# Kernel tuning notes

Hardware: AMD Instinct MI355X
Metric: run time of the kernel (lower is better)

## Reference

```python
import jax, jax.numpy as jnp
import numpy as np

NUM_HEADS = 6
WIN = 16
NW = 16   # number of windows sharing one mask (b_ % NW == 0)


def setup_inputs() -> dict:
    key = jax.random.key(0)
    ks = jax.random.split(key, 6)
    b_, n, dim = 256, WIN * WIN, 192
    qkv = jax.random.normal(ks[0], (b_, n, 3 * dim), dtype=jnp.float32)
    rpi = jax.random.randint(ks[1], (n, n), 0, (2 * WIN - 1) * (2 * WIN - 1))
    # additive attention mask per window-group (Swin uses 0 / -100; randn is fine for math)
    mask = jax.random.normal(ks[2], (NW, n, n), dtype=jnp.float32)
    rpb_table = 0.02 * jax.random.normal(ks[3], ((2 * WIN - 1) * (2 * WIN - 1), NUM_HEADS), dtype=jnp.float32)
    proj_w = jax.random.normal(ks[4], (dim, dim), dtype=jnp.float32) * (1.0 / np.sqrt(dim))
    proj_b = jax.random.normal(ks[5], (dim,), dtype=jnp.float32) * 0.01
    return {"qkv": qkv, "rpi": rpi, "mask": mask, "rpb_table": rpb_table,
            "proj_w": proj_w, "proj_b": proj_b}


def reference(qkv, rpi, mask, rpb_table, proj_w, proj_b):
    b_, n, c3 = qkv.shape
    c = c3 // 3
    h = NUM_HEADS
    hd = c // h
    scale = float(hd) ** -0.5
    # (b_, n, 3, h, hd) -> (3, b_, h, n, hd)
    qkv = qkv.reshape(b_, n, 3, h, hd).transpose(2, 0, 3, 1, 4)
    q, k, v = qkv[0] * scale, qkv[1], qkv[2]
    attn = jnp.einsum('bhqd,bhkd->bhqk', q, k)  # [b_, h, n, n]
    # gathered relative position bias: [n, n, h] -> [h, n, n]
    bias = rpb_table[rpi].transpose(2, 0, 1)
    attn = attn + bias[None]
    # add per-window-group mask: [b_//nw, nw, h, n, n]
    nw = mask.shape[0]
    attn = attn.reshape(b_ // nw, nw, h, n, n) + mask[None, :, None]
    attn = attn.reshape(b_, h, n, n)
    attn = jax.nn.softmax(attn, axis=-1)
    x = jnp.einsum('bhqk,bhkd->bhqd', attn, v)  # [b_, h, n, hd]
    x = x.transpose(0, 2, 1, 3).reshape(b_, n, c)
    # nn.Linear: x @ W^T + b
    return x @ proj_w.T + proj_b
```

## Files before the change

### kernel.cpp

```cpp
#include <hip/hip_runtime.h>
#include <hip/hip_bf16.h>

typedef _Float16 f16;
typedef _Float16 f16x2 __attribute__((ext_vector_type(2)));
typedef _Float16 f16x4 __attribute__((ext_vector_type(4)));
typedef _Float16 f16x8 __attribute__((ext_vector_type(8)));
typedef __fp16 h16x2 __attribute__((ext_vector_type(2)));
typedef float f32x4 __attribute__((ext_vector_type(4)));

#define NHEADS 6
#define NTOK 256
#define NWINS 256
#define DIM 192
#define HD 32
#define C3 576
#define LOG2E 1.4426950408889634f
#define SCALE (0.17677669529663687f * LOG2E)

__device__ inline f16x2 pkrtz(float a, float b) {
  h16x2 r = __builtin_amdgcn_cvt_pkrtz(a, b);
  return __builtin_bit_cast(f16x2, r);
}

__global__ __launch_bounds__(256) void prep_cb_kernel(const int* __restrict__ rpi,
                                                      const float* __restrict__ mask,
                                                      const float* __restrict__ rpb,
                                                      f16* __restrict__ cb) {
  int idx = blockIdx.x * 256 + threadIdx.x;
  int k = idx & 255;
  int q = (idx >> 8) & 255;
  int t = idx >> 16;
  int h = t % 6;
  int mg = t / 6;
  float v = (rpb[rpi[(q << 8) | k] * 6 + h] + mask[(mg << 16) | (q << 8) | k]) * LOG2E;
  cb[idx] = (f16)v;
}

__global__ __launch_bounds__(256) void prep_w_kernel(const float* __restrict__ w,
                                                     f16* __restrict__ w16) {
  int i = blockIdx.x * 256 + threadIdx.x;
  if (i < DIM * DIM) w16[i] = (f16)w[i];
}

__device__ inline f16x8 q_to_f16(float4 a, float4 b) {
  f16x2 p0 = pkrtz(a.x * SCALE, a.y * SCALE);
  f16x2 p1 = pkrtz(a.z * SCALE, a.w * SCALE);
  f16x2 p2 = pkrtz(b.x * SCALE, b.y * SCALE);
  f16x2 p3 = pkrtz(b.z * SCALE, b.w * SCALE);
  f16x4 lo = __builtin_shufflevector(p0, p1, 0, 1, 2, 3);
  f16x4 hi = __builtin_shufflevector(p2, p3, 0, 1, 2, 3);
  return __builtin_shufflevector(lo, hi, 0, 1, 2, 3, 4, 5, 6, 7);
}

__global__ __launch_bounds__(256, 4) void attn_kernel(const float* __restrict__ qkv,
                                                      const f16* __restrict__ cb,
                                                      f16* __restrict__ x16) {
  const int idx = blockIdx.x;
  const int b = idx & 255;
  const int h = idx >> 8;
  const int tid = threadIdx.x;
  const int lane = tid & 63;
  const int wave = tid >> 6;
  const int g = lane >> 4;
  const int r16 = lane & 15;

  __shared__ f16 Klin[16 * 64 * 8];
  __shared__ f16 VT[32][264];

  const int qbase = wave * 64;
  const size_t cb_base = ((size_t)((b & 15) * 6 + h)) << 16;
  const f16* cbp = cb + cb_base + ((size_t)(qbase + r16) << 8) + g * 4;

  const int srow = tid >> 3;
  const int part = tid & 7;
  const float* kbase = qkv + (size_t)(b * NTOK + srow) * C3 + DIM + h * HD + part * 4;
  float4 ka[4], va[4], kb[4], vb[4];
#pragma unroll
  for (int rg = 0; rg < 4; ++rg) {
    const float* kp = kbase + (size_t)(rg * 32) * C3;
    ka[rg] = *(const float4*)kp;
    va[rg] = *(const float4*)(kp + DIM);
  }
#pragma unroll
  for (int rg = 0; rg < 4; ++rg) {
    const float* kp = kbase + (size_t)(rg * 32 + 128) * C3;
    kb[rg] = *(const float4*)kp;
    vb[rg] = *(const float4*)(kp + DIM);
  }

  f16x4 cvA[8], cvB[8];
#pragma unroll
  for (int i = 0; i < 8; ++i) cvA[i] = *((const f16x4*)(cbp + i * 16));

  const float* qp = qkv + (size_t)(b * NTOK + qbase + r16) * C3 + h * HD + g * 8;
  float4 qn0 = ((const float4*)qp)[0];
  float4 qn1 = ((const float4*)qp)[1];

  const int gg = part >> 1;
  const int half = part & 1;
  const int d0 = part * 4;
#pragma unroll
  for (int rg = 0; rg < 4; ++rg) {
    const int row = rg * 32 + srow;
    const int slot = ((row >> 4) * 64) + gg * 16 + ((row & 15) ^ (gg << 2));
    f16x2 k01 = pkrtz(ka[rg].x, ka[rg].y);
    f16x2 k23 = pkrtz(ka[rg].z, ka[rg].w);
    *((f16x4*)&Klin[slot * 8 + half * 4]) = __builtin_shufflevector(k01, k23, 0, 1, 2, 3);
    VT[d0 + 0][row ^ (((d0 + 0) & 7) << 2)] = (f16)va[rg].x;
    VT[d0 + 1][row ^ (((d0 + 1) & 7) << 2)] = (f16)va[rg].y;
    VT[d0 + 2][row ^ (((d0 + 2) & 7) << 2)] = (f16)va[rg].z;
    VT[d0 + 3][row ^ (((d0 + 3) & 7) << 2)] = (f16)va[rg].w;
  }
#pragma unroll
  for (int rg = 0; rg < 4; ++rg) {
    const int row = rg * 32 + srow + 128;
    const int slot = ((row >> 4) * 64) + gg * 16 + ((row & 15) ^ (gg << 2));
    f16x2 k01 = pkrtz(kb[rg].x, kb[rg].y);
    f16x2 k23 = pkrtz(kb[rg].z, kb[rg].w);
    *((f16x4*)&Klin[slot * 8 + half * 4]) = __builtin_shufflevector(k01, k23, 0, 1, 2, 3);
    VT[d0 + 0][row ^ (((d0 + 0) & 7) << 2)] = (f16)vb[rg].x;
    VT[d0 + 1][row ^ (((d0 + 1) & 7) << 2)] = (f16)vb[rg].y;
    VT[d0 + 2][row ^ (((d0 + 2) & 7) << 2)] = (f16)vb[rg].z;
    VT[d0 + 3][row ^ (((d0 + 3) & 7) << 2)] = (f16)vb[rg].w;
  }

  f16x8 qf = q_to_f16(qn0, qn1);

  __syncthreads();

  const int krd = (lane & 48) + ((lane & 15) ^ ((lane >> 2) & 12));

#pragma unroll
  for (int c = 0; c < 4; ++c) {
    f32x4 acc[8];
#pragma unroll
    for (int kt = 0; kt < 8; ++kt) {
      acc[kt][0] = 0.f; acc[kt][1] = 0.f; acc[kt][2] = 0.f; acc[kt][3] = 0.f;
    }
#pragma unroll
    for (int kt = 0; kt < 8; ++kt) {
      f16x8 af = *((const f16x8*)&Klin[(kt * 64 + krd) * 8]);
      acc[kt] = __builtin_amdgcn_mfma_f32_16x16x32_f16(af, qf, acc[kt], 0, 0, 0);
    }

    const f16* cbc = cbp + c * 4096;
#pragma unroll
    for (int i = 0; i < 8; ++i) cvB[i] = *((const f16x4*)(cbc + (8 + i) * 16));

    float m0 = -1e30f, m1 = -1e30f, m2 = -1e30f, m3 = -1e30f;
#pragma unroll
    for (int kt = 0; kt < 8; ++kt) {
      acc[kt][0] += (float)cvA[kt][0];
      acc[kt][1] += (float)cvA[kt][1];
      acc[kt][2] += (float)cvA[kt][2];
      acc[kt][3] += (float)cvA[kt][3];
      m0 = fmaxf(m0, acc[kt][0]);
      m1 = fmaxf(m1, acc[kt][1]);
      m2 = fmaxf(m2, acc[kt][2]);
      m3 = fmaxf(m3, acc[kt][3]);
    }
    float mA = fmaxf(fmaxf(m0, m1), fmaxf(m2, m3));
    mA = fmaxf(mA, __shfl_xor(mA, 16));
    mA = fmaxf(mA, __shfl_xor(mA, 32));

    float s0 = 0.f, s1 = 0.f, s2 = 0.f, s3 = 0.f;
#pragma unroll
    for (int kt = 0; kt < 8; ++kt) {
      float p0 = __builtin_amdgcn_exp2f(acc[kt][0] - mA);
      float p1 = __builtin_amdgcn_exp2f(acc[kt][1] - mA);
      float p2 = __builtin_amdgcn_exp2f(acc[kt][2] - mA);
      float p3 = __builtin_amdgcn_exp2f(acc[kt][3] - mA);
      acc[kt][0] = p0; acc[kt][1] = p1; acc[kt][2] = p2; acc[kt][3] = p3;
      s0 += p0; s1 += p1; s2 += p2; s3 += p3;
    }
    float sA = (s0 + s1) + (s2 + s3);

    f32x4 xacc[2];
    xacc[0][0] = 0.f; xacc[0][1] = 0.f; xacc[0][2] = 0.f; xacc[0][3] = 0.f;
    xacc[1][0] = 0.f; xacc[1][1] = 0.f; xacc[1][2] = 0.f; xacc[1][3] = 0.f;
#pragma unroll
    for (int kt = 0; kt < 8; ++kt) {
      f16x2 p01 = pkrtz(acc[kt][0], acc[kt][1]);
      f16x2 p23 = pkrtz(acc[kt][2], acc[kt][3]);
      f16x4 pf = __builtin_shufflevector(p01, p23, 0, 1, 2, 3);
#pragma unroll
      for (int dt = 0; dt < 2; ++dt) {
        const int col = (kt * 16 + g * 4) ^ ((r16 & 7) << 2);
        f16x4 vf = *((const f16x4*)&VT[dt * 16 + r16][col]);
        xacc[dt] = __builtin_amdgcn_mfma_f32_16x16x16f16(vf, pf, xacc[dt], 0, 0, 0);
      }
    }

#pragma unroll
    for (int kt = 0; kt < 8; ++kt) {
      acc[kt][0] = 0.f; acc[kt][1] = 0.f; acc[kt][2] = 0.f; acc[kt][3] = 0.f;
    }
#pragma unroll
    for (int kt = 0; kt < 8; ++kt) {
      f16x8 af = *((const f16x8*)&Klin[((kt + 8) * 64 + krd) * 8]);
      acc[kt] = __builtin_amdgcn_mfma_f32_16x16x32_f16(af, qf, acc[kt], 0, 0, 0);
    }

    if (c < 3) {
#pragma unroll
      for (int i = 0; i < 8; ++i) cvA[i] = *((const f16x4*)(cbc + 4096 + i * 16));
      const float* qpn = qp + (size_t)((c + 1) * 16) * C3;
      qn0 = ((const float4*)qpn)[0];
      qn1 = ((const float4*)qpn)[1];
    }

    m0 = -1e30f; m1 = -1e30f; m2 = -1e30f; m3 = -1e30f;
#pragma unroll
    for (int kt = 0; kt < 8; ++kt) {
      acc[kt][0] += (float)cvB[kt][0];
      acc[kt][1] += (float)cvB[kt][1];
      acc[kt][2] += (float)cvB[kt][2];
      acc[kt][3] += (float)cvB[kt][3];
      m0 = fmaxf(m0, acc[kt][0]);
      m1 = fmaxf(m1, acc[kt][1]);
      m2 = fmaxf(m2, acc[kt][2]);
      m3 = fmaxf(m3, acc[kt][3]);
    }
    float mB = fmaxf(fmaxf(m0, m1), fmaxf(m2, m3));
    mB = fmaxf(mB, __shfl_xor(mB, 16));
    mB = fmaxf(mB, __shfl_xor(mB, 32));

    const float m = fmaxf(mA, mB);
    const float scA = __builtin_amdgcn_exp2f(mA - m);

    s0 = 0.f; s1 = 0.f; s2 = 0.f; s3 = 0.f;
#pragma unroll
    for (int kt = 0; kt < 8; ++kt) {
      float p0 = __builtin_amdgcn_exp2f(acc[kt][0] - m);
      float p1 = __builtin_amdgcn_exp2f(acc[kt][1] - m);
      float p2 = __builtin_amdgcn_exp2f(acc[kt][2] - m);
      float p3 = __builtin_amdgcn_exp2f(acc[kt][3] - m);
      acc[kt][0] = p0; acc[kt][1] = p1; acc[kt][2] = p2; acc[kt][3] = p3;
      s0 += p0; s1 += p1; s2 += p2; s3 += p3;
    }
    float s = sA * scA + (s0 + s1) + (s2 + s3);
    s += __shfl_xor(s, 16);
    s += __shfl_xor(s, 32);
    const float rinv = 1.0f / s;

    xacc[0][0] *= scA; xacc[0][1] *= scA; xacc[0][2] *= scA; xacc[0][3] *= scA;
    xacc[1][0] *= scA; xacc[1][1] *= scA; xacc[1][2] *= scA; xacc[1][3] *= scA;
#pragma unroll
    for (int kt = 0; kt < 8; ++kt) {
      f16x2 p01 = pkrtz(acc[kt][0], acc[kt][1]);
      f16x2 p23 = pkrtz(acc[kt][2], acc[kt][3]);
      f16x4 pf = __builtin_shufflevector(p01, p23, 0, 1, 2, 3);
#pragma unroll
      for (int dt = 0; dt < 2; ++dt) {
        const int col = ((kt + 8) * 16 + g * 4) ^ ((r16 & 7) << 2);
        f16x4 vf = *((const f16x4*)&VT[dt * 16 + r16][col]);
        xacc[dt] = __builtin_amdgcn_mfma_f32_16x16x16f16(vf, pf, xacc[dt], 0, 0, 0);
      }
    }

    f16* xp = x16 + (size_t)(b * NTOK + qbase + c * 16 + r16) * DIM + h * HD;
#pragma unroll
    for (int dt = 0; dt < 2; ++dt) {
      f16x2 o01 = pkrtz(xacc[dt][0] * rinv, xacc[dt][1] * rinv);
      f16x2 o23 = pkrtz(xacc[dt][2] * rinv, xacc[dt][3] * rinv);
      *((f16x4*)(xp + dt * 16 + g * 4)) = __builtin_shufflevector(o01, o23, 0, 1, 2, 3);
    }

    if (c < 3) qf = q_to_f16(qn0, qn1);
  }
}

__global__ __launch_bounds__(256) void proj_kernel(const f16* __restrict__ x16,
                                                   const f16* __restrict__ w16,
                                                   const float* __restrict__ pb,
                                                   float* __restrict__ out) {
  const int lane = threadIdx.x & 63;
  const int wave = threadIdx.x >> 6;
  const int g = lane >> 4;
  const int r16 = lane & 15;
  const int m0 = blockIdx.x * 64 + wave * 16;

  f32x4 acc[12];
#pragma unroll
  for (int jt = 0; jt < 12; ++jt) {
    acc[jt][0] = 0.f; acc[jt][1] = 0.f; acc[jt][2] = 0.f; acc[jt][3] = 0.f;
  }
#pragma unroll
  for (int cc = 0; cc < 6; ++cc) {
    f16x8 af = *((const f16x8*)(x16 + (size_t)(m0 + r16) * DIM + cc * 32 + g * 8));
#pragma unroll
    for (int jt = 0; jt < 12; ++jt) {
      f16x8 bf = *((const f16x8*)(w16 + (size_t)(jt * 16 + r16) * DIM + cc * 32 + g * 8));
      acc[jt] = __builtin_amdgcn_mfma_f32_16x16x32_f16(af, bf, acc[jt], 0, 0, 0);
    }
  }
#pragma unroll
  for (int jt = 0; jt < 12; ++jt) {
    int j = jt * 16 + r16;
    float bias = pb[j];
#pragma unroll
    for (int r = 0; r < 4; ++r) {
      out[(size_t)(m0 + g * 4 + r) * DIM + j] = acc[jt][r] + bias;
    }
  }
}

extern "C" void kernel_launch(void* const* d_in, const int* in_sizes, int n_in,
                              void* d_out, int out_size, void* d_ws, size_t ws_size,
                              hipStream_t stream) {
  const float* qkv  = (const float*)d_in[0];
  const int*   rpi  = (const int*)d_in[1];
  const float* mask = (const float*)d_in[2];
  const float* rpb  = (const float*)d_in[3];
  const float* pw   = (const float*)d_in[4];
  const float* pbv  = (const float*)d_in[5];
  float* out = (float*)d_out;

  char* ws = (char*)d_ws;
  f16* cb  = (f16*)ws;
  f16* x16 = (f16*)(ws + 12582912);
  f16* w16 = (f16*)(ws + 12582912 + 25165824);

  prep_cb_kernel<<<24576, 256, 0, stream>>>(rpi, mask, rpb, cb);
  prep_w_kernel<<<144, 256, 0, stream>>>(pw, w16);
  attn_kernel<<<1536, 256, 0, stream>>>(qkv, cb, x16);
  proj_kernel<<<1024, 256, 0, stream>>>(x16, w16, pbv, out);
}
```

Baseline: 120.0 us.

## Use 512-thread attention blocks, fp32 bias table preloaded into MFMA accumulators

Doubles the attention block to 512 threads (8 waves), so each wave handles 32 query rows instead of 64, and splits the K and V staging between the two halves of the block. The combined bias/mask table is now stored in fp32 and loaded straight into the MFMA accumulators as their initial value, which removes the separate add pass after the QK^T product. This doubles the bias table's global memory footprint and traffic and drops the prefetch of the next chunk's bias and Q. The aim is more waves in flight and fewer ALU instructions per score.

```diff
diff --git a/kernel.cpp b/kernel.cpp
--- a/kernel.cpp
+++ b/kernel.cpp
@@ -25,15 +25,14 @@
 __global__ __launch_bounds__(256) void prep_cb_kernel(const int* __restrict__ rpi,
                                                       const float* __restrict__ mask,
                                                       const float* __restrict__ rpb,
-                                                      f16* __restrict__ cb) {
+                                                      float* __restrict__ cb) {
   int idx = blockIdx.x * 256 + threadIdx.x;
   int k = idx & 255;
   int q = (idx >> 8) & 255;
   int t = idx >> 16;
   int h = t % 6;
   int mg = t / 6;
-  float v = (rpb[rpi[(q << 8) | k] * 6 + h] + mask[(mg << 16) | (q << 8) | k]) * LOG2E;
-  cb[idx] = (f16)v;
+  cb[idx] = (rpb[rpi[(q << 8) | k] * 6 + h] + mask[(mg << 16) | (q << 8) | k]) * LOG2E;
 }
 
 __global__ __launch_bounds__(256) void prep_w_kernel(const float* __restrict__ w,
@@ -52,8 +51,8 @@
   return __builtin_shufflevector(lo, hi, 0, 1, 2, 3, 4, 5, 6, 7);
 }
 
-__global__ __launch_bounds__(256, 4) void attn_kernel(const float* __restrict__ qkv,
-                                                      const f16* __restrict__ cb,
+__global__ __launch_bounds__(512, 8) void attn_kernel(const float* __restrict__ qkv,
+                                                      const float* __restrict__ cb,
                                                       f16* __restrict__ x16) {
   const int idx = blockIdx.x;
   const int b = idx & 255;
@@ -67,97 +66,71 @@
   __shared__ f16 Klin[16 * 64 * 8];
   __shared__ f16 VT[32][264];
 
-  const int qbase = wave * 64;
-  const size_t cb_base = ((size_t)((b & 15) * 6 + h)) << 16;
-  const f16* cbp = cb + cb_base + ((size_t)(qbase + r16) << 8) + g * 4;
-
-  const int srow = tid >> 3;
-  const int part = tid & 7;
-  const float* kbase = qkv + (size_t)(b * NTOK + srow) * C3 + DIM + h * HD + part * 4;
-  float4 ka[4], va[4], kb[4], vb[4];
-#pragma unroll
-  for (int rg = 0; rg < 4; ++rg) {
-    const float* kp = kbase + (size_t)(rg * 32) * C3;
-    ka[rg] = *(const float4*)kp;
-    va[rg] = *(const float4*)(kp + DIM);
-  }
-#pragma unroll
-  for (int rg = 0; rg < 4; ++rg) {
-    const float* kp = kbase + (size_t)(rg * 32 + 128) * C3;
-    kb[rg] = *(const float4*)kp;
-    vb[rg] = *(const float4*)(kp + DIM);
-  }
-
-  f16x4 cvA[8], cvB[8];
-#pragma unroll
-  for (int i = 0; i < 8; ++i) cvA[i] = *((const f16x4*)(cbp + i * 16));
-
-  const float* qp = qkv + (size_t)(b * NTOK + qbase + r16) * C3 + h * HD + g * 8;
-  float4 qn0 = ((const float4*)qp)[0];
-  float4 qn1 = ((const float4*)qp)[1];
-
-  const int gg = part >> 1;
-  const int half = part & 1;
-  const int d0 = part * 4;
-#pragma unroll
-  for (int rg = 0; rg < 4; ++rg) {
-    const int row = rg * 32 + srow;
-    const int slot = ((row >> 4) * 64) + gg * 16 + ((row & 15) ^ (gg << 2));
-    f16x2 k01 = pkrtz(ka[rg].x, ka[rg].y);
-    f16x2 k23 = pkrtz(ka[rg].z, ka[rg].w);
-    *((f16x4*)&Klin[slot * 8 + half * 4]) = __builtin_shufflevector(k01, k23, 0, 1, 2, 3);
-    VT[d0 + 0][row ^ (((d0 + 0) & 7) << 2)] = (f16)va[rg].x;
-    VT[d0 + 1][row ^ (((d0 + 1) & 7) << 2)] = (f16)va[rg].y;
-    VT[d0 + 2][row ^ (((d0 + 2) & 7) << 2)] = (f16)va[rg].z;
-    VT[d0 + 3][row ^ (((d0 + 3) & 7) << 2)] = (f16)va[rg].w;
-  }
-#pragma unroll
-  for (int rg = 0; rg < 4; ++rg) {
-    const int row = rg * 32 + srow + 128;
-    const int slot = ((row >> 4) * 64) + gg * 16 + ((row & 15) ^ (gg << 2));
-    f16x2 k01 = pkrtz(kb[rg].x, kb[rg].y);
-    f16x2 k23 = pkrtz(kb[rg].z, kb[rg].w);
-    *((f16x4*)&Klin[slot * 8 + half * 4]) = __builtin_shufflevector(k01, k23, 0, 1, 2, 3);
-    VT[d0 + 0][row ^ (((d0 + 0) & 7) << 2)] = (f16)vb[rg].x;
-    VT[d0 + 1][row ^ (((d0 + 1) & 7) << 2)] = (f16)vb[rg].y;
-    VT[d0 + 2][row ^ (((d0 + 2) & 7) << 2)] = (f16)vb[rg].z;
-    VT[d0 + 3][row ^ (((d0 + 3) & 7) << 2)] = (f16)vb[rg].w;
-  }
-
-  f16x8 qf = q_to_f16(qn0, qn1);
-
+  {
+    const int t = tid & 255;
+    const int srow = t >> 3;
+    const int part = t & 7;
+    const bool isK = tid < 256;
+    const float* base = qkv + (size_t)(b * NTOK + srow) * C3 + DIM + (isK ? 0 : DIM)
+                        + h * HD + part * 4;
+    const int gg = part >> 1;
+    const int half = part & 1;
+    const int d0 = part * 4;
+#pragma unroll
+    for (int batch = 0; batch < 2; ++batch) {
+      float4 v4[4];
+#pragma unroll
+      for (int rg = 0; rg < 4; ++rg)
+        v4[rg] = *(const float4*)(base + (size_t)((batch * 4 + rg) * 32) * C3);
+#pragma unroll
+      for (int rg = 0; rg < 4; ++rg) {
+        const int row = (batch * 4 + rg) * 32 + srow;
+        if (isK) {
+          const int slot = ((row >> 4) * 64) + gg * 16 + ((row & 15) ^ (gg << 2));
+          f16x2 k01 = pkrtz(v4[rg].x, v4[rg].y);
+          f16x2 k23 = pkrtz(v4[rg].z, v4[rg].w);
+          *((f16x4*)&Klin[slot * 8 + half * 4]) =
+              __builtin_shufflevector(k01, k23, 0, 1, 2, 3);
+        } else {
+          VT[d0 + 0][row ^ (((d0 + 0) & 7) << 2)] = (f16)v4[rg].x;
+          VT[d0 + 1][row ^ (((d0 + 1) & 7) << 2)] = (f16)v4[rg].y;
+          VT[d0 + 2][row ^ (((d0 + 2) & 7) << 2)] = (f16)v4[rg].z;
+          VT[d0 + 3][row ^ (((d0 + 3) & 7) << 2)] = (f16)v4[rg].w;
+        }
+      }
+    }
+  }
   __syncthreads();
 
+  const int qbase = wave * 32;
+  const float* cbb = cb + (((size_t)((b & 15) * 6 + h)) << 16);
   const int krd = (lane & 48) + ((lane & 15) ^ ((lane >> 2) & 12));
 
 #pragma unroll
-  for (int c = 0; c < 4; ++c) {
+  for (int c = 0; c < 2; ++c) {
+    const int qrow = qbase + c * 16 + r16;
+    const float* qp = qkv + (size_t)(b * NTOK + qrow) * C3 + h * HD + g * 8;
+    f16x8 qf = q_to_f16(((const float4*)qp)[0], ((const float4*)qp)[1]);
+    const float* cbq = cbb + ((size_t)qrow << 8) + g * 4;
+
     f32x4 acc[8];
 #pragma unroll
-    for (int kt = 0; kt < 8; ++kt) {
-      acc[kt][0] = 0.f; acc[kt][1] = 0.f; acc[kt][2] = 0.f; acc[kt][3] = 0.f;
-    }
+    for (int kt = 0; kt < 8; ++kt)
+      acc[kt] = *((const f32x4*)(cbq + kt * 16));
 #pragma unroll
     for (int kt = 0; kt < 8; ++kt) {
       f16x8 af = *((const f16x8*)&Klin[(kt * 64 + krd) * 8]);
       acc[kt] = __builtin_amdgcn_mfma_f32_16x16x32_f16(af, qf, acc[kt], 0, 0, 0);
     }
 
-    const f16* cbc = cbp + c * 4096;
-#pragma unroll
-    for (int i = 0; i < 8; ++i) cvB[i] = *((const f16x4*)(cbc + (8 + i) * 16));
-
-    float m0 = -1e30f, m1 = -1e30f, m2 = -1e30f, m3 = -1e30f;
-#pragma unroll
-    for (int kt = 0; kt < 8; ++kt) {
-      acc[kt][0] += (float)cvA[kt][0];
-      acc[kt][1] += (float)cvA[kt][1];
-      acc[kt][2] += (float)cvA[kt][2];
-      acc[kt][3] += (float)cvA[kt][3];
-      m0 = fmaxf(m0, acc[kt][0]);
-      m1 = fmaxf(m1, acc[kt][1]);
-      m2 = fmaxf(m2, acc[kt][2]);
-      m3 = fmaxf(m3, acc[kt][3]);
+    float m0 = fmaxf(fmaxf(acc[0][0], acc[1][0]), fmaxf(acc[2][0], acc[3][0]));
+    float m1 = fmaxf(fmaxf(acc[0][1], acc[1][1]), fmaxf(acc[2][1], acc[3][1]));
+    float m2 = fmaxf(fmaxf(acc[0][2], acc[1][2]), fmaxf(acc[2][2], acc[3][2]));
+    float m3 = fmaxf(fmaxf(acc[0][3], acc[1][3]), fmaxf(acc[2][3], acc[3][3]));
+#pragma unroll
+    for (int kt = 4; kt < 8; ++kt) {
+      m0 = fmaxf(m0, acc[kt][0]); m1 = fmaxf(m1, acc[kt][1]);
+      m2 = fmaxf(m2, acc[kt][2]); m3 = fmaxf(m3, acc[kt][3]);
     }
     float mA = fmaxf(fmaxf(m0, m1), fmaxf(m2, m3));
     mA = fmaxf(mA, __shfl_xor(mA, 16));
@@ -192,34 +165,22 @@
     }
 
 #pragma unroll
-    for (int kt = 0; kt < 8; ++kt) {
-      acc[kt][0] = 0.f; acc[kt][1] = 0.f; acc[kt][2] = 0.f; acc[kt][3] = 0.f;
-    }
+    for (int kt = 0; kt < 8; ++kt)
+      acc[kt] = *((const f32x4*)(cbq + 128 + kt * 16));
 #pragma unroll
     for (int kt = 0; kt < 8; ++kt) {
       f16x8 af = *((const f16x8*)&Klin[((kt + 8) * 64 + krd) * 8]);
       acc[kt] = __builtin_amdgcn_mfma_f32_16x16x32_f16(af, qf, acc[kt], 0, 0, 0);
     }
 
-    if (c < 3) {
-#pragma unroll
-      for (int i = 0; i < 8; ++i) cvA[i] = *((const f16x4*)(cbc + 4096 + i * 16));
-      const float* qpn = qp + (size_t)((c + 1) * 16) * C3;
-      qn0 = ((const float4*)qpn)[0];
-      qn1 = ((const float4*)qpn)[1];
-    }
-
-    m0 = -1e30f; m1 = -1e30f; m2 = -1e30f; m3 = -1e30f;
-#pragma unroll
-    for (int kt = 0; kt < 8; ++kt) {
-      acc[kt][0] += (float)cvB[kt][0];
-      acc[kt][1] += (float)cvB[kt][1];
-      acc[kt][2] += (float)cvB[kt][2];
-      acc[kt][3] += (float)cvB[kt][3];
-      m0 = fmaxf(m0, acc[kt][0]);
-      m1 = fmaxf(m1, acc[kt][1]);
-      m2 = fmaxf(m2, acc[kt][2]);
-      m3 = fmaxf(m3, acc[kt][3]);
+    m0 = fmaxf(fmaxf(acc[0][0], acc[1][0]), fmaxf(acc[2][0], acc[3][0]));
+    m1 = fmaxf(fmaxf(acc[0][1], acc[1][1]), fmaxf(acc[2][1], acc[3][1]));
+    m2 = fmaxf(fmaxf(acc[0][2], acc[1][2]), fmaxf(acc[2][2], acc[3][2]));
+    m3 = fmaxf(fmaxf(acc[0][3], acc[1][3]), fmaxf(acc[2][3], acc[3][3]));
+#pragma unroll
+    for (int kt = 4; kt < 8; ++kt) {
+      m0 = fmaxf(m0, acc[kt][0]); m1 = fmaxf(m1, acc[kt][1]);
+      m2 = fmaxf(m2, acc[kt][2]); m3 = fmaxf(m3, acc[kt][3]);
     }
     float mB = fmaxf(fmaxf(m0, m1), fmaxf(m2, m3));
     mB = fmaxf(mB, __shfl_xor(mB, 16));
@@ -258,15 +219,13 @@
       }
     }
 
-    f16* xp = x16 + (size_t)(b * NTOK + qbase + c * 16 + r16) * DIM + h * HD;
+    f16* xp = x16 + (size_t)(b * NTOK + qrow) * DIM + h * HD;
 #pragma unroll
     for (int dt = 0; dt < 2; ++dt) {
       f16x2 o01 = pkrtz(xacc[dt][0] * rinv, xacc[dt][1] * rinv);
       f16x2 o23 = pkrtz(xacc[dt][2] * rinv, xacc[dt][3] * rinv);
       *((f16x4*)(xp + dt * 16 + g * 4)) = __builtin_shufflevector(o01, o23, 0, 1, 2, 3);
     }
-
-    if (c < 3) qf = q_to_f16(qn0, qn1);
   }
 }
 
@@ -317,12 +276,12 @@
   float* out = (float*)d_out;
 
   char* ws = (char*)d_ws;
-  f16* cb  = (f16*)ws;
-  f16* x16 = (f16*)(ws + 12582912);
-  f16* w16 = (f16*)(ws + 12582912 + 25165824);
+  float* cb = (float*)ws;
+  f16* x16  = (f16*)(ws + 25165824);
+  f16* w16  = (f16*)(ws + 25165824 + 25165824);
 
   prep_cb_kernel<<<24576, 256, 0, stream>>>(rpi, mask, rpb, cb);
   prep_w_kernel<<<144, 256, 0, stream>>>(pw, w16);
-  attn_kernel<<<1536, 256, 0, stream>>>(qkv, cb, x16);
+  attn_kernel<<<1536, 512, 0, stream>>>(qkv, cb, x16);
   proj_kernel<<<1024, 256, 0, stream>>>(x16, w16, pbv, out);
 }
```

Result: slower. 195.1 us (+62.7%).
